# Performance work log

Measured on AMD Instinct MI355X. Metric: run time of the kernel, lower is better.

Reference implementation:

```python
import jax, jax.numpy as jnp
import numpy as np

NEG_BIG = -1.0e9


def setup_inputs() -> dict:
    key = jax.random.key(0)
    ks = jax.random.split(key, 8)
    B, N, D = 4, 384, 256
    s = 1.0 / np.sqrt(D)
    return {
        "q": jax.random.normal(ks[0], (B, N, D), dtype=jnp.float32),
        "k": jax.random.normal(ks[1], (B, N, D), dtype=jnp.float32),
        "v": jax.random.normal(ks[2], (B, N, D), dtype=jnp.float32),
        "mask": jax.random.randint(ks[3], (B, 1, N, N), 0, 2, dtype=jnp.int32),
        "Wq": jax.random.normal(ks[4], (D, D), dtype=jnp.float32) * s,
        "bq": jnp.zeros((D,), dtype=jnp.float32),
        "Wk": jax.random.normal(ks[5], (D, D), dtype=jnp.float32) * s,
        "bk": jnp.zeros((D,), dtype=jnp.float32),
        "Wv": jax.random.normal(ks[6], (D, D), dtype=jnp.float32) * s,
        "bv": jnp.zeros((D,), dtype=jnp.float32),
    }


def reference(q, k, v, mask, Wq, bq, Wk, bk, Wv, bv):
    # Dense projections
    query = q @ Wq + bq   # [B, N, D]
    key_p = k @ Wk + bk   # [B, M, D]
    value = v @ Wv + bv   # [B, M, D]
    # Per-channel outer-product scores: [B, D, N, M]
    score = jnp.einsum('bnd,bmd->bdnm', query, key_p)
    score = score + mask.astype(score.dtype) * NEG_BIG  # mask broadcasts [B,1,N,M]
    weights = jnp.tanh(score)
    # Per-channel weighted sum back to [B, N, D]
    out = jnp.einsum('bdnm,bmd->bnd', weights, value)
    return out
```

## Files before the change

kernel.cpp:

```cpp
#include <hip/hip_runtime.h>

#define DD 256
#define NN 384
#define BB 4
#define BN (BB * NN)
#define MSPLIT 8
#define MCHUNK (NN / MSPLIT)
#define ROWS 8
#define PSTRIDE (BN * DD)

constexpr float TWO_LOG2E = 2.8853900817779268f;
constexpr float MASK_X    = -1.0e9f * 2.8853900817779268f;

__global__ __launch_bounds__(256) void proj_kernel(
    const float* __restrict__ q,  const float* __restrict__ k,  const float* __restrict__ v,
    const float* __restrict__ Wq, const float* __restrict__ Wk, const float* __restrict__ Wv,
    const float* __restrict__ bq, const float* __restrict__ bk, const float* __restrict__ bv,
    float* __restrict__ Qout, float* __restrict__ KVout)
{
    const int tid  = threadIdx.x;
    const int lane = tid & 63;
    const int wv   = tid >> 6;
    const int row  = blockIdx.x * 8 + wv * 2;
    const int which = blockIdx.y;

    const float* X; const float* W; const float* bias; float scale; float* out; int ostride;
    if (which == 0)      { X = q; W = Wq; bias = bq; scale = 1.0f;      out = Qout;      ostride = 1; }
    else if (which == 1) { X = k; W = Wk; bias = bk; scale = TWO_LOG2E; out = KVout;     ostride = 2; }
    else                 { X = v; W = Wv; bias = bv; scale = 1.0f;      out = KVout + 1; ostride = 2; }

    const float* X0 = X + (size_t)row * DD;
    const float* X1 = X0 + DD;
    const float* Wp = W + lane * 4;

    float4 a0 = make_float4(0.f, 0.f, 0.f, 0.f);
    float4 a1 = make_float4(0.f, 0.f, 0.f, 0.f);

    #pragma unroll 2
    for (int kk = 0; kk < DD; kk += 4) {
        const float4 x0 = *reinterpret_cast<const float4*>(X0 + kk);
        const float4 x1 = *reinterpret_cast<const float4*>(X1 + kk);
        const float4 w0 = *reinterpret_cast<const float4*>(Wp + (size_t)(kk + 0) * DD);
        const float4 w1 = *reinterpret_cast<const float4*>(Wp + (size_t)(kk + 1) * DD);
        const float4 w2 = *reinterpret_cast<const float4*>(Wp + (size_t)(kk + 2) * DD);
        const float4 w3 = *reinterpret_cast<const float4*>(Wp + (size_t)(kk + 3) * DD);

        a0.x = fmaf(x0.x, w0.x, a0.x); a0.y = fmaf(x0.x, w0.y, a0.y);
        a0.z = fmaf(x0.x, w0.z, a0.z); a0.w = fmaf(x0.x, w0.w, a0.w);
        a1.x = fmaf(x1.x, w0.x, a1.x); a1.y = fmaf(x1.x, w0.y, a1.y);
        a1.z = fmaf(x1.x, w0.z, a1.z); a1.w = fmaf(x1.x, w0.w, a1.w);

        a0.x = fmaf(x0.y, w1.x, a0.x); a0.y = fmaf(x0.y, w1.y, a0.y);
        a0.z = fmaf(x0.y, w1.z, a0.z); a0.w = fmaf(x0.y, w1.w, a0.w);
        a1.x = fmaf(x1.y, w1.x, a1.x); a1.y = fmaf(x1.y, w1.y, a1.y);
        a1.z = fmaf(x1.y, w1.z, a1.z); a1.w = fmaf(x1.y, w1.w, a1.w);

        a0.x = fmaf(x0.z, w2.x, a0.x); a0.y = fmaf(x0.z, w2.y, a0.y);
        a0.z = fmaf(x0.z, w2.z, a0.z); a0.w = fmaf(x0.z, w2.w, a0.w);
        a1.x = fmaf(x1.z, w2.x, a1.x); a1.y = fmaf(x1.z, w2.y, a1.y);
        a1.z = fmaf(x1.z, w2.z, a1.z); a1.w = fmaf(x1.z, w2.w, a1.w);

        a0.x = fmaf(x0.w, w3.x, a0.x); a0.y = fmaf(x0.w, w3.y, a0.y);
        a0.z = fmaf(x0.w, w3.z, a0.z); a0.w = fmaf(x0.w, w3.w, a0.w);
        a1.x = fmaf(x1.w, w3.x, a1.x); a1.y = fmaf(x1.w, w3.y, a1.y);
        a1.z = fmaf(x1.w, w3.z, a1.z); a1.w = fmaf(x1.w, w3.w, a1.w);
    }

    const float4 bb = *reinterpret_cast<const float4*>(bias + lane * 4);
    const float r0x = (a0.x + bb.x) * scale, r0y = (a0.y + bb.y) * scale;
    const float r0z = (a0.z + bb.z) * scale, r0w = (a0.w + bb.w) * scale;
    const float r1x = (a1.x + bb.x) * scale, r1y = (a1.y + bb.y) * scale;
    const float r1z = (a1.z + bb.z) * scale, r1w = (a1.w + bb.w) * scale;

    if (ostride == 1) {
        *reinterpret_cast<float4*>(out + (size_t)row * DD + lane * 4)
            = make_float4(r0x, r0y, r0z, r0w);
        *reinterpret_cast<float4*>(out + (size_t)(row + 1) * DD + lane * 4)
            = make_float4(r1x, r1y, r1z, r1w);
    } else {
        float* o0 = out + ((size_t)row * DD + lane * 4) * 2;
        float* o1 = out + ((size_t)(row + 1) * DD + lane * 4) * 2;
        o0[0] = r0x; o0[2] = r0y; o0[4] = r0z; o0[6] = r0w;
        o1[0] = r1x; o1[2] = r1y; o1[4] = r1z; o1[6] = r1w;
    }
}

__global__ __launch_bounds__(256) void mhsa_kernel(
    const float* __restrict__ Q, const float* __restrict__ KV,
    const int* __restrict__ mask, float* __restrict__ outp)
{
    const int tid = threadIdx.x;
    const int b   = blockIdx.y;
    const int n0  = blockIdx.x * ROWS;
    const int m0  = blockIdx.z * MCHUNK;

    __shared__ float mf[MCHUNK][ROWS];
    for (int idx = tid; idx < MCHUNK * ROWS; idx += 256) {
        const int m = idx % MCHUNK;
        const int j = idx / MCHUNK;
        mf[m][j] = mask[(size_t)(b * NN + n0 + j) * NN + (m0 + m)] ? MASK_X : 0.0f;
    }
    __syncthreads();

    const float* Qp = Q + (size_t)(b * NN + n0) * DD + tid;
    float qv0 = Qp[0 * DD], qv1 = Qp[1 * DD], qv2 = Qp[2 * DD], qv3 = Qp[3 * DD];
    float qv4 = Qp[4 * DD], qv5 = Qp[5 * DD], qv6 = Qp[6 * DD], qv7 = Qp[7 * DD];

    const float2* kvp = reinterpret_cast<const float2*>(KV)
                      + (size_t)b * NN * DD + (size_t)m0 * DD + tid;

    float acc0 = 0.f, acc1 = 0.f, acc2 = 0.f, acc3 = 0.f;
    float acc4 = 0.f, acc5 = 0.f, acc6 = 0.f, acc7 = 0.f, vsum = 0.f;

#define TANH1(ACC, XV, T2) \
    ACC = fmaf(T2, __builtin_amdgcn_rcpf(__builtin_amdgcn_exp2f(XV) + 1.0f), ACC);

#define COMP(KVV, MLOC)                                                        \
    {                                                                          \
        const float4 ma = *reinterpret_cast<const float4*>(&mf[MLOC][0]);      \
        const float4 mb = *reinterpret_cast<const float4*>(&mf[MLOC][4]);      \
        const float kk = (KVV).x, vv = (KVV).y;                                \
        const float t2 = -2.0f * vv;                                           \
        vsum += vv;                                                            \
        TANH1(acc0, fmaf(qv0, kk, ma.x), t2)                                   \
        TANH1(acc1, fmaf(qv1, kk, ma.y), t2)                                   \
        TANH1(acc2, fmaf(qv2, kk, ma.z), t2)                                   \
        TANH1(acc3, fmaf(qv3, kk, ma.w), t2)                                   \
        TANH1(acc4, fmaf(qv4, kk, mb.x), t2)                                   \
        TANH1(acc5, fmaf(qv5, kk, mb.y), t2)                                   \
        TANH1(acc6, fmaf(qv6, kk, mb.z), t2)                                   \
        TANH1(acc7, fmaf(qv7, kk, mb.w), t2)                                   \
    }

#define LOADG(B0, B1, B2, B3, M0)                \
    B0 = kvp[(size_t)((M0) + 0) * DD];           \
    B1 = kvp[(size_t)((M0) + 1) * DD];           \
    B2 = kvp[(size_t)((M0) + 2) * DD];           \
    B3 = kvp[(size_t)((M0) + 3) * DD];

    float2 A0, A1, A2, A3, B0, B1, B2, B3;
    LOADG(A0, A1, A2, A3, 0)
    LOADG(B0, B1, B2, B3, 4)

    for (int mg = 0; mg < MCHUNK; mg += 8) {
        COMP(A0, mg + 0) COMP(A1, mg + 1) COMP(A2, mg + 2) COMP(A3, mg + 3)
        LOADG(A0, A1, A2, A3, mg + 8)
        COMP(B0, mg + 4) COMP(B1, mg + 5) COMP(B2, mg + 6) COMP(B3, mg + 7)
        LOADG(B0, B1, B2, B3, mg + 12)
    }
#undef COMP
#undef TANH1
#undef LOADG

    float* po = outp + (size_t)blockIdx.z * PSTRIDE + (size_t)(b * NN + n0) * DD + tid;
    po[0 * DD] = acc0 + vsum; po[1 * DD] = acc1 + vsum;
    po[2 * DD] = acc2 + vsum; po[3 * DD] = acc3 + vsum;
    po[4 * DD] = acc4 + vsum; po[5 * DD] = acc5 + vsum;
    po[6 * DD] = acc6 + vsum; po[7 * DD] = acc7 + vsum;
}

__global__ __launch_bounds__(256) void reduce8_kernel(
    const float* __restrict__ part, float* __restrict__ out)
{
    const int i = blockIdx.x * 256 + threadIdx.x;
    float s0 = part[i + 0 * PSTRIDE] + part[i + 1 * PSTRIDE];
    float s1 = part[i + 2 * PSTRIDE] + part[i + 3 * PSTRIDE];
    float s2 = part[i + 4 * PSTRIDE] + part[i + 5 * PSTRIDE];
    float s3 = part[i + 6 * PSTRIDE] + part[i + 7 * PSTRIDE];
    out[i] = (s0 + s1) + (s2 + s3);
}

extern "C" void kernel_launch(void* const* d_in, const int* in_sizes, int n_in,
                              void* d_out, int out_size, void* d_ws, size_t ws_size,
                              hipStream_t stream) {
    const float* q    = (const float*)d_in[0];
    const float* k    = (const float*)d_in[1];
    const float* v    = (const float*)d_in[2];
    const int*   mask = (const int*)  d_in[3];
    const float* Wq   = (const float*)d_in[4];
    const float* bq   = (const float*)d_in[5];
    const float* Wk   = (const float*)d_in[6];
    const float* bk   = (const float*)d_in[7];
    const float* Wv   = (const float*)d_in[8];
    const float* bv   = (const float*)d_in[9];
    float* out = (float*)d_out;

    float* Qws   = (float*)d_ws;
    float* KVws  = Qws  + (size_t)BN * DD;
    float* Pws   = KVws + (size_t)2 * BN * DD;

    dim3 g1(BN / 8, 3);
    proj_kernel<<<g1, 256, 0, stream>>>(q, k, v, Wq, Wk, Wv, bq, bk, bv, Qws, KVws);

    dim3 g2(NN / ROWS, BB, MSPLIT);
    mhsa_kernel<<<g2, 256, 0, stream>>>(Qws, KVws, mask, Pws);

    reduce8_kernel<<<dim3(BN * DD / 256), 256, 0, stream>>>(Pws, out);
}
```

Before: 146.7 us.

## Restructure projection with split-K LDS tiles and halve attention M-split

The projection kernel now stages four input rows in shared memory and splits the K dimension across two waves. Each thread accumulates four rows with software-prefetched weight loads, and the two partial sums are combined through LDS before bias and scale are applied. The attention kernel's M split drops from 8 to 4, so fewer partial outputs are written and the final reduction reads four slices instead of eight. The trade-off is less parallelism in the main kernel, with 384 instead of 768 blocks and twice the serial M work per block.

```diff
diff --git a/kernel.cpp b/kernel.cpp
--- a/kernel.cpp
+++ b/kernel.cpp
@@ -4,7 +4,7 @@
 #define NN 384
 #define BB 4
 #define BN (BB * NN)
-#define MSPLIT 8
+#define MSPLIT 4
 #define MCHUNK (NN / MSPLIT)
 #define ROWS 8
 #define PSTRIDE (BN * DD)
@@ -12,7 +12,7 @@
 constexpr float TWO_LOG2E = 2.8853900817779268f;
 constexpr float MASK_X    = -1.0e9f * 2.8853900817779268f;
 
-__global__ __launch_bounds__(256) void proj_kernel(
+__global__ __launch_bounds__(128, 2) void proj_kernel(
     const float* __restrict__ q,  const float* __restrict__ k,  const float* __restrict__ v,
     const float* __restrict__ Wq, const float* __restrict__ Wk, const float* __restrict__ Wv,
     const float* __restrict__ bq, const float* __restrict__ bk, const float* __restrict__ bv,
@@ -21,7 +21,7 @@
     const int tid  = threadIdx.x;
     const int lane = tid & 63;
     const int wv   = tid >> 6;
-    const int row  = blockIdx.x * 8 + wv * 2;
+    const int row0 = blockIdx.x * 4;
     const int which = blockIdx.y;
 
     const float* X; const float* W; const float* bias; float scale; float* out; int ostride;
@@ -29,59 +29,69 @@
     else if (which == 1) { X = k; W = Wk; bias = bk; scale = TWO_LOG2E; out = KVout;     ostride = 2; }
     else                 { X = v; W = Wv; bias = bv; scale = 1.0f;      out = KVout + 1; ostride = 2; }
 
-    const float* X0 = X + (size_t)row * DD;
-    const float* X1 = X0 + DD;
-    const float* Wp = W + lane * 4;
-
-    float4 a0 = make_float4(0.f, 0.f, 0.f, 0.f);
-    float4 a1 = make_float4(0.f, 0.f, 0.f, 0.f);
-
-    #pragma unroll 2
-    for (int kk = 0; kk < DD; kk += 4) {
-        const float4 x0 = *reinterpret_cast<const float4*>(X0 + kk);
-        const float4 x1 = *reinterpret_cast<const float4*>(X1 + kk);
-        const float4 w0 = *reinterpret_cast<const float4*>(Wp + (size_t)(kk + 0) * DD);
-        const float4 w1 = *reinterpret_cast<const float4*>(Wp + (size_t)(kk + 1) * DD);
-        const float4 w2 = *reinterpret_cast<const float4*>(Wp + (size_t)(kk + 2) * DD);
-        const float4 w3 = *reinterpret_cast<const float4*>(Wp + (size_t)(kk + 3) * DD);
-
-        a0.x = fmaf(x0.x, w0.x, a0.x); a0.y = fmaf(x0.x, w0.y, a0.y);
-        a0.z = fmaf(x0.x, w0.z, a0.z); a0.w = fmaf(x0.x, w0.w, a0.w);
-        a1.x = fmaf(x1.x, w0.x, a1.x); a1.y = fmaf(x1.x, w0.y, a1.y);
-        a1.z = fmaf(x1.x, w0.z, a1.z); a1.w = fmaf(x1.x, w0.w, a1.w);
-
-        a0.x = fmaf(x0.y, w1.x, a0.x); a0.y = fmaf(x0.y, w1.y, a0.y);
-        a0.z = fmaf(x0.y, w1.z, a0.z); a0.w = fmaf(x0.y, w1.w, a0.w);
-        a1.x = fmaf(x1.y, w1.x, a1.x); a1.y = fmaf(x1.y, w1.y, a1.y);
-        a1.z = fmaf(x1.y, w1.z, a1.z); a1.w = fmaf(x1.y, w1.w, a1.w);
-
-        a0.x = fmaf(x0.z, w2.x, a0.x); a0.y = fmaf(x0.z, w2.y, a0.y);
-        a0.z = fmaf(x0.z, w2.z, a0.z); a0.w = fmaf(x0.z, w2.w, a0.w);
-        a1.x = fmaf(x1.z, w2.x, a1.x); a1.y = fmaf(x1.z, w2.y, a1.y);
-        a1.z = fmaf(x1.z, w2.z, a1.z); a1.w = fmaf(x1.z, w2.w, a1.w);
-
-        a0.x = fmaf(x0.w, w3.x, a0.x); a0.y = fmaf(x0.w, w3.y, a0.y);
-        a0.z = fmaf(x0.w, w3.z, a0.z); a0.w = fmaf(x0.w, w3.w, a0.w);
-        a1.x = fmaf(x1.w, w3.x, a1.x); a1.y = fmaf(x1.w, w3.y, a1.y);
-        a1.z = fmaf(x1.w, w3.z, a1.z); a1.w = fmaf(x1.w, w3.w, a1.w);
-    }
-
-    const float4 bb = *reinterpret_cast<const float4*>(bias + lane * 4);
-    const float r0x = (a0.x + bb.x) * scale, r0y = (a0.y + bb.y) * scale;
-    const float r0z = (a0.z + bb.z) * scale, r0w = (a0.w + bb.w) * scale;
-    const float r1x = (a1.x + bb.x) * scale, r1y = (a1.y + bb.y) * scale;
-    const float r1z = (a1.z + bb.z) * scale, r1w = (a1.w + bb.w) * scale;
-
-    if (ostride == 1) {
-        *reinterpret_cast<float4*>(out + (size_t)row * DD + lane * 4)
-            = make_float4(r0x, r0y, r0z, r0w);
-        *reinterpret_cast<float4*>(out + (size_t)(row + 1) * DD + lane * 4)
-            = make_float4(r1x, r1y, r1z, r1w);
-    } else {
-        float* o0 = out + ((size_t)row * DD + lane * 4) * 2;
-        float* o1 = out + ((size_t)(row + 1) * DD + lane * 4) * 2;
-        o0[0] = r0x; o0[2] = r0y; o0[4] = r0z; o0[6] = r0w;
-        o1[0] = r1x; o1[2] = r1y; o1[4] = r1z; o1[6] = r1w;
+    __shared__ float xs[4][DD];
+    __shared__ float ps[2][4][DD];
+
+    for (int e = tid; e < 4 * DD; e += 128)
+        xs[e >> 8][e & 255] = X[(size_t)(row0 + (e >> 8)) * DD + (e & 255)];
+    __syncthreads();
+
+    const int k0 = wv * 128;
+    const float* Wp = W + (size_t)k0 * DD + lane * 4;
+
+    float4 acc0 = make_float4(0.f,0.f,0.f,0.f), acc1 = acc0, acc2 = acc0, acc3 = acc0;
+
+#define LDG(G, WD0, WD1, WD2, WD3, XD0, XD1, XD2, XD3)                         \
+    WD0 = *reinterpret_cast<const float4*>(Wp + (size_t)((G) * 4 + 0) * DD);   \
+    WD1 = *reinterpret_cast<const float4*>(Wp + (size_t)((G) * 4 + 1) * DD);   \
+    WD2 = *reinterpret_cast<const float4*>(Wp + (size_t)((G) * 4 + 2) * DD);   \
+    WD3 = *reinterpret_cast<const float4*>(Wp + (size_t)((G) * 4 + 3) * DD);   \
+    XD0 = *reinterpret_cast<const float4*>(&xs[0][k0 + (G) * 4]);              \
+    XD1 = *reinterpret_cast<const float4*>(&xs[1][k0 + (G) * 4]);              \
+    XD2 = *reinterpret_cast<const float4*>(&xs[2][k0 + (G) * 4]);              \
+    XD3 = *reinterpret_cast<const float4*>(&xs[3][k0 + (G) * 4]);
+
+#define FMA4(ACC, X4, W0, W1, W2, W3)                                          \
+    ACC.x = fmaf(X4.x, W0.x, ACC.x); ACC.y = fmaf(X4.x, W0.y, ACC.y);          \
+    ACC.z = fmaf(X4.x, W0.z, ACC.z); ACC.w = fmaf(X4.x, W0.w, ACC.w);          \
+    ACC.x = fmaf(X4.y, W1.x, ACC.x); ACC.y = fmaf(X4.y, W1.y, ACC.y);          \
+    ACC.z = fmaf(X4.y, W1.z, ACC.z); ACC.w = fmaf(X4.y, W1.w, ACC.w);          \
+    ACC.x = fmaf(X4.z, W2.x, ACC.x); ACC.y = fmaf(X4.z, W2.y, ACC.y);          \
+    ACC.z = fmaf(X4.z, W2.z, ACC.z); ACC.w = fmaf(X4.z, W2.w, ACC.w);          \
+    ACC.x = fmaf(X4.w, W3.x, ACC.x); ACC.y = fmaf(X4.w, W3.y, ACC.y);          \
+    ACC.z = fmaf(X4.w, W3.z, ACC.z); ACC.w = fmaf(X4.w, W3.w, ACC.w);
+
+    float4 wA0, wA1, wA2, wA3, xA0, xA1, xA2, xA3;
+    float4 wB0, wB1, wB2, wB3, xB0, xB1, xB2, xB3;
+    LDG(0, wA0, wA1, wA2, wA3, xA0, xA1, xA2, xA3)
+    LDG(1, wB0, wB1, wB2, wB3, xB0, xB1, xB2, xB3)
+
+    for (int g = 0; g < 32; g += 2) {
+        FMA4(acc0, xA0, wA0, wA1, wA2, wA3)
+        FMA4(acc1, xA1, wA0, wA1, wA2, wA3)
+        FMA4(acc2, xA2, wA0, wA1, wA2, wA3)
+        FMA4(acc3, xA3, wA0, wA1, wA2, wA3)
+        LDG((g + 2) & 31, wA0, wA1, wA2, wA3, xA0, xA1, xA2, xA3)
+        FMA4(acc0, xB0, wB0, wB1, wB2, wB3)
+        FMA4(acc1, xB1, wB0, wB1, wB2, wB3)
+        FMA4(acc2, xB2, wB0, wB1, wB2, wB3)
+        FMA4(acc3, xB3, wB0, wB1, wB2, wB3)
+        LDG((g + 3) & 31, wB0, wB1, wB2, wB3, xB0, xB1, xB2, xB3)
+    }
+#undef LDG
+#undef FMA4
+
+    *reinterpret_cast<float4*>(&ps[wv][0][lane * 4]) = acc0;
+    *reinterpret_cast<float4*>(&ps[wv][1][lane * 4]) = acc1;
+    *reinterpret_cast<float4*>(&ps[wv][2][lane * 4]) = acc2;
+    *reinterpret_cast<float4*>(&ps[wv][3][lane * 4]) = acc3;
+    __syncthreads();
+
+    for (int e = tid; e < 4 * DD; e += 128) {
+        const int r = e >> 8;
+        const int d = e & 255;
+        const float s = ps[0][r][d] + ps[1][r][d];
+        out[((size_t)(row0 + r) * DD + d) * ostride] = (s + bias[d]) * scale;
     }
 }
 
@@ -159,15 +169,12 @@
     po[6 * DD] = acc6 + vsum; po[7 * DD] = acc7 + vsum;
 }
 
-__global__ __launch_bounds__(256) void reduce8_kernel(
+__global__ __launch_bounds__(256) void reduce4_kernel(
     const float* __restrict__ part, float* __restrict__ out)
 {
     const int i = blockIdx.x * 256 + threadIdx.x;
-    float s0 = part[i + 0 * PSTRIDE] + part[i + 1 * PSTRIDE];
-    float s1 = part[i + 2 * PSTRIDE] + part[i + 3 * PSTRIDE];
-    float s2 = part[i + 4 * PSTRIDE] + part[i + 5 * PSTRIDE];
-    float s3 = part[i + 6 * PSTRIDE] + part[i + 7 * PSTRIDE];
-    out[i] = (s0 + s1) + (s2 + s3);
+    out[i] = (part[i] + part[i + PSTRIDE])
+           + (part[i + 2 * PSTRIDE] + part[i + 3 * PSTRIDE]);
 }
 
 extern "C" void kernel_launch(void* const* d_in, const int* in_sizes, int n_in,
@@ -189,11 +196,11 @@
     float* KVws  = Qws  + (size_t)BN * DD;
     float* Pws   = KVws + (size_t)2 * BN * DD;
 
-    dim3 g1(BN / 8, 3);
-    proj_kernel<<<g1, 256, 0, stream>>>(q, k, v, Wq, Wk, Wv, bq, bk, bv, Qws, KVws);
+    dim3 g1(BN / 4, 3);
+    proj_kernel<<<g1, 128, 0, stream>>>(q, k, v, Wq, Wk, Wv, bq, bk, bv, Qws, KVws);
 
     dim3 g2(NN / ROWS, BB, MSPLIT);
     mhsa_kernel<<<g2, 256, 0, stream>>>(Qws, KVws, mask, Pws);
 
-    reduce8_kernel<<<dim3(BN * DD / 256), 256, 0, stream>>>(Pws, out);
-}
+    reduce4_kernel<<<dim3(BN * DD / 256), 256, 0, stream>>>(Pws, out);
+}
```

Measured after the change: 157.3 us. 7.2% more time.

## Split projection GEMM over K with partial planes and separate bias reduce

Applied to the files above, without the earlier changes.

The projection kernel is restructured to split the 256-long reduction into four chunks. Each block stages its 4 input rows in shared memory and accumulates 4 rows by 2 columns per thread, which gives more blocks and smaller per-thread work. A new reduce kernel sums the four partial planes, adds the bias, applies the key scaling and interleaves K/V. The trade-off is an extra kernel launch and extra global traffic for writing and re-reading the partials.

```diff
diff --git a/kernel.cpp b/kernel.cpp
--- a/kernel.cpp
+++ b/kernel.cpp
@@ -7,82 +7,93 @@
 #define MSPLIT 8
 #define MCHUNK (NN / MSPLIT)
 #define ROWS 8
-#define PSTRIDE (BN * DD)
+#define KSPLIT 4
+#define KCH (DD / KSPLIT)
+#define QP (BN * DD)
+#define PLANE (3 * QP)
 
 constexpr float TWO_LOG2E = 2.8853900817779268f;
 constexpr float MASK_X    = -1.0e9f * 2.8853900817779268f;
 
-__global__ __launch_bounds__(256) void proj_kernel(
+__global__ __launch_bounds__(128) void proj_kernel(
     const float* __restrict__ q,  const float* __restrict__ k,  const float* __restrict__ v,
     const float* __restrict__ Wq, const float* __restrict__ Wk, const float* __restrict__ Wv,
+    float* __restrict__ Pp)
+{
+    const int tid   = threadIdx.x;
+    const int row0  = blockIdx.x * 4;
+    const int which = blockIdx.y;
+    const int k0    = blockIdx.z * KCH;
+
+    const float* X = (which == 0) ? q  : (which == 1) ? k  : v;
+    const float* W = (which == 0) ? Wq : (which == 1) ? Wk : Wv;
+
+    __shared__ float xs[4][KCH];
+    {
+        const int e0 = tid;
+        xs[e0 >> 6][e0 & 63] = X[(size_t)(row0 + (e0 >> 6)) * DD + k0 + (e0 & 63)];
+        const int e1 = tid + 128;
+        xs[e1 >> 6][e1 & 63] = X[(size_t)(row0 + (e1 >> 6)) * DD + k0 + (e1 & 63)];
+    }
+    __syncthreads();
+
+    const float* Wp = W + (size_t)k0 * DD + tid * 2;
+
+    float2 a0{0.f,0.f}, a1{0.f,0.f}, a2{0.f,0.f}, a3{0.f,0.f};
+
+    #pragma unroll 2
+    for (int g = 0; g < KCH; g += 4) {
+        const float2 w0 = *reinterpret_cast<const float2*>(Wp + (size_t)(g + 0) * DD);
+        const float2 w1 = *reinterpret_cast<const float2*>(Wp + (size_t)(g + 1) * DD);
+        const float2 w2 = *reinterpret_cast<const float2*>(Wp + (size_t)(g + 2) * DD);
+        const float2 w3 = *reinterpret_cast<const float2*>(Wp + (size_t)(g + 3) * DD);
+        const float4 x0 = *reinterpret_cast<const float4*>(&xs[0][g]);
+        const float4 x1 = *reinterpret_cast<const float4*>(&xs[1][g]);
+        const float4 x2 = *reinterpret_cast<const float4*>(&xs[2][g]);
+        const float4 x3 = *reinterpret_cast<const float4*>(&xs[3][g]);
+
+        a0.x = fmaf(x0.x, w0.x, a0.x); a0.y = fmaf(x0.x, w0.y, a0.y);
+        a1.x = fmaf(x1.x, w0.x, a1.x); a1.y = fmaf(x1.x, w0.y, a1.y);
+        a2.x = fmaf(x2.x, w0.x, a2.x); a2.y = fmaf(x2.x, w0.y, a2.y);
+        a3.x = fmaf(x3.x, w0.x, a3.x); a3.y = fmaf(x3.x, w0.y, a3.y);
+
+        a0.x = fmaf(x0.y, w1.x, a0.x); a0.y = fmaf(x0.y, w1.y, a0.y);
+        a1.x = fmaf(x1.y, w1.x, a1.x); a1.y = fmaf(x1.y, w1.y, a1.y);
+        a2.x = fmaf(x2.y, w1.x, a2.x); a2.y = fmaf(x2.y, w1.y, a2.y);
+        a3.x = fmaf(x3.y, w1.x, a3.x); a3.y = fmaf(x3.y, w1.y, a3.y);
+
+        a0.x = fmaf(x0.z, w2.x, a0.x); a0.y = fmaf(x0.z, w2.y, a0.y);
+        a1.x = fmaf(x1.z, w2.x, a1.x); a1.y = fmaf(x1.z, w2.y, a1.y);
+        a2.x = fmaf(x2.z, w2.x, a2.x); a2.y = fmaf(x2.z, w2.y, a2.y);
+        a3.x = fmaf(x3.z, w2.x, a3.x); a3.y = fmaf(x3.z, w2.y, a3.y);
+
+        a0.x = fmaf(x0.w, w3.x, a0.x); a0.y = fmaf(x0.w, w3.y, a0.y);
+        a1.x = fmaf(x1.w, w3.x, a1.x); a1.y = fmaf(x1.w, w3.y, a1.y);
+        a2.x = fmaf(x2.w, w3.x, a2.x); a2.y = fmaf(x2.w, w3.y, a2.y);
+        a3.x = fmaf(x3.w, w3.x, a3.x); a3.y = fmaf(x3.w, w3.y, a3.y);
+    }
+
+    float* o = Pp + (size_t)blockIdx.z * PLANE + (size_t)which * QP
+             + (size_t)row0 * DD + tid * 2;
+    *reinterpret_cast<float2*>(o + 0 * DD) = a0;
+    *reinterpret_cast<float2*>(o + 1 * DD) = a1;
+    *reinterpret_cast<float2*>(o + 2 * DD) = a2;
+    *reinterpret_cast<float2*>(o + 3 * DD) = a3;
+}
+
+__global__ __launch_bounds__(256) void preduce_kernel(
+    const float* __restrict__ Pp,
     const float* __restrict__ bq, const float* __restrict__ bk, const float* __restrict__ bv,
     float* __restrict__ Qout, float* __restrict__ KVout)
 {
-    const int tid  = threadIdx.x;
-    const int lane = tid & 63;
-    const int wv   = tid >> 6;
-    const int row  = blockIdx.x * 8 + wv * 2;
     const int which = blockIdx.y;
-
-    const float* X; const float* W; const float* bias; float scale; float* out; int ostride;
-    if (which == 0)      { X = q; W = Wq; bias = bq; scale = 1.0f;      out = Qout;      ostride = 1; }
-    else if (which == 1) { X = k; W = Wk; bias = bk; scale = TWO_LOG2E; out = KVout;     ostride = 2; }
-    else                 { X = v; W = Wv; bias = bv; scale = 1.0f;      out = KVout + 1; ostride = 2; }
-
-    const float* X0 = X + (size_t)row * DD;
-    const float* X1 = X0 + DD;
-    const float* Wp = W + lane * 4;
-
-    float4 a0 = make_float4(0.f, 0.f, 0.f, 0.f);
-    float4 a1 = make_float4(0.f, 0.f, 0.f, 0.f);
-
-    #pragma unroll 2
-    for (int kk = 0; kk < DD; kk += 4) {
-        const float4 x0 = *reinterpret_cast<const float4*>(X0 + kk);
-        const float4 x1 = *reinterpret_cast<const float4*>(X1 + kk);
-        const float4 w0 = *reinterpret_cast<const float4*>(Wp + (size_t)(kk + 0) * DD);
-        const float4 w1 = *reinterpret_cast<const float4*>(Wp + (size_t)(kk + 1) * DD);
-        const float4 w2 = *reinterpret_cast<const float4*>(Wp + (size_t)(kk + 2) * DD);
-        const float4 w3 = *reinterpret_cast<const float4*>(Wp + (size_t)(kk + 3) * DD);
-
-        a0.x = fmaf(x0.x, w0.x, a0.x); a0.y = fmaf(x0.x, w0.y, a0.y);
-        a0.z = fmaf(x0.x, w0.z, a0.z); a0.w = fmaf(x0.x, w0.w, a0.w);
-        a1.x = fmaf(x1.x, w0.x, a1.x); a1.y = fmaf(x1.x, w0.y, a1.y);
-        a1.z = fmaf(x1.x, w0.z, a1.z); a1.w = fmaf(x1.x, w0.w, a1.w);
-
-        a0.x = fmaf(x0.y, w1.x, a0.x); a0.y = fmaf(x0.y, w1.y, a0.y);
-        a0.z = fmaf(x0.y, w1.z, a0.z); a0.w = fmaf(x0.y, w1.w, a0.w);
-        a1.x = fmaf(x1.y, w1.x, a1.x); a1.y = fmaf(x1.y, w1.y, a1.y);
-        a1.z = fmaf(x1.y, w1.z, a1.z); a1.w = fmaf(x1.y, w1.w, a1.w);
-
-        a0.x = fmaf(x0.z, w2.x, a0.x); a0.y = fmaf(x0.z, w2.y, a0.y);
-        a0.z = fmaf(x0.z, w2.z, a0.z); a0.w = fmaf(x0.z, w2.w, a0.w);
-        a1.x = fmaf(x1.z, w2.x, a1.x); a1.y = fmaf(x1.z, w2.y, a1.y);
-        a1.z = fmaf(x1.z, w2.z, a1.z); a1.w = fmaf(x1.z, w2.w, a1.w);
-
-        a0.x = fmaf(x0.w, w3.x, a0.x); a0.y = fmaf(x0.w, w3.y, a0.y);
-        a0.z = fmaf(x0.w, w3.z, a0.z); a0.w = fmaf(x0.w, w3.w, a0.w);
-        a1.x = fmaf(x1.w, w3.x, a1.x); a1.y = fmaf(x1.w, w3.y, a1.y);
-        a1.z = fmaf(x1.w, w3.z, a1.z); a1.w = fmaf(x1.w, w3.w, a1.w);
-    }
-
-    const float4 bb = *reinterpret_cast<const float4*>(bias + lane * 4);
-    const float r0x = (a0.x + bb.x) * scale, r0y = (a0.y + bb.y) * scale;
-    const float r0z = (a0.z + bb.z) * scale, r0w = (a0.w + bb.w) * scale;
-    const float r1x = (a1.x + bb.x) * scale, r1y = (a1.y + bb.y) * scale;
-    const float r1z = (a1.z + bb.z) * scale, r1w = (a1.w + bb.w) * scale;
-
-    if (ostride == 1) {
-        *reinterpret_cast<float4*>(out + (size_t)row * DD + lane * 4)
-            = make_float4(r0x, r0y, r0z, r0w);
-        *reinterpret_cast<float4*>(out + (size_t)(row + 1) * DD + lane * 4)
-            = make_float4(r1x, r1y, r1z, r1w);
-    } else {
-        float* o0 = out + ((size_t)row * DD + lane * 4) * 2;
-        float* o1 = out + ((size_t)(row + 1) * DD + lane * 4) * 2;
-        o0[0] = r0x; o0[2] = r0y; o0[4] = r0z; o0[6] = r0w;
-        o1[0] = r1x; o1[2] = r1y; o1[4] = r1z; o1[6] = r1w;
-    }
+    const int i = blockIdx.x * 256 + threadIdx.x;
+    const float* p = Pp + (size_t)which * QP + i;
+    const float s = (p[0] + p[(size_t)PLANE]) + (p[2 * (size_t)PLANE] + p[3 * (size_t)PLANE]);
+    const int d = i & 255;
+    if (which == 0)      Qout[i]          = s + bq[d];
+    else if (which == 1) KVout[2 * i]     = (s + bk[d]) * TWO_LOG2E;
+    else                 KVout[2 * i + 1] = s + bv[d];
 }
 
 __global__ __launch_bounds__(256) void mhsa_kernel(
@@ -152,7 +163,7 @@
 #undef TANH1
 #undef LOADG
 
-    float* po = outp + (size_t)blockIdx.z * PSTRIDE + (size_t)(b * NN + n0) * DD + tid;
+    float* po = outp + (size_t)blockIdx.z * QP + (size_t)(b * NN + n0) * DD + tid;
     po[0 * DD] = acc0 + vsum; po[1 * DD] = acc1 + vsum;
     po[2 * DD] = acc2 + vsum; po[3 * DD] = acc3 + vsum;
     po[4 * DD] = acc4 + vsum; po[5 * DD] = acc5 + vsum;
@@ -163,10 +174,10 @@
     const float* __restrict__ part, float* __restrict__ out)
 {
     const int i = blockIdx.x * 256 + threadIdx.x;
-    float s0 = part[i + 0 * PSTRIDE] + part[i + 1 * PSTRIDE];
-    float s1 = part[i + 2 * PSTRIDE] + part[i + 3 * PSTRIDE];
-    float s2 = part[i + 4 * PSTRIDE] + part[i + 5 * PSTRIDE];
-    float s3 = part[i + 6 * PSTRIDE] + part[i + 7 * PSTRIDE];
+    float s0 = part[i + 0 * (size_t)QP] + part[i + 1 * (size_t)QP];
+    float s1 = part[i + 2 * (size_t)QP] + part[i + 3 * (size_t)QP];
+    float s2 = part[i + 4 * (size_t)QP] + part[i + 5 * (size_t)QP];
+    float s3 = part[i + 6 * (size_t)QP] + part[i + 7 * (size_t)QP];
     out[i] = (s0 + s1) + (s2 + s3);
 }
 
@@ -185,15 +196,19 @@
     const float* bv   = (const float*)d_in[9];
     float* out = (float*)d_out;
 
-    float* Qws   = (float*)d_ws;
-    float* KVws  = Qws  + (size_t)BN * DD;
-    float* Pws   = KVws + (size_t)2 * BN * DD;
-
-    dim3 g1(BN / 8, 3);
-    proj_kernel<<<g1, 256, 0, stream>>>(q, k, v, Wq, Wk, Wv, bq, bk, bv, Qws, KVws);
-
-    dim3 g2(NN / ROWS, BB, MSPLIT);
-    mhsa_kernel<<<g2, 256, 0, stream>>>(Qws, KVws, mask, Pws);
-
-    reduce8_kernel<<<dim3(BN * DD / 256), 256, 0, stream>>>(Pws, out);
-}
+    float* Qws  = (float*)d_ws;
+    float* KVws = Qws  + (size_t)QP;
+    float* Pp   = KVws + (size_t)2 * QP;
+    float* Pm   = Pp   + (size_t)KSPLIT * PLANE;
+
+    proj_kernel<<<dim3(BN / 4, 3, KSPLIT), 128, 0, stream>>>(
+        q, k, v, Wq, Wk, Wv, Pp);
+
+    preduce_kernel<<<dim3(QP / 256, 3), 256, 0, stream>>>(
+        Pp, bq, bk, bv, Qws, KVws);
+
+    mhsa_kernel<<<dim3(NN / ROWS, BB, MSPLIT), 256, 0, stream>>>(
+        Qws, KVws, mask, Pm);
+
+    reduce8_kernel<<<dim3(QP / 256), 256, 0, stream>>>(Pm, out);
+}
```

Measured after the change: 137.7 us. 1.07x faster.
